# Kernel optimization log

Hardware: AMD Instinct MI355X
Metric: run time of the kernel (lower is better)

The kernel has to match this reference:

```python
import jax, jax.numpy as jnp
import numpy as np

B, N, K, D, H, L = 2, 2048, 256, 768, 256, 64
REL_PROP = 3
NUM_BUCKETS = 64


def _pair_scores(u, dist_feat, left_w, left_b, right_w, right_b, out_w, out_b):
    # OptFFpairs-style pairwise scorer: left(u)_i + right(u)_j + dist_emb -> relu -> out
    left = jnp.einsum('bkd,hd->bkh', u, left_w) + left_b    # [B,K,H]
    right = jnp.einsum('bkd,hd->bkh', u, right_w) + right_b  # [B,K,H]
    h = jax.nn.relu(left[:, :, None, :] + right[:, None, :, :] + dist_feat)  # [B,K,K,H]
    return jnp.einsum('bijh,lh->bijl', h, out_w) + out_b     # [B,K,K,L]


def setup_inputs():
    key = jax.random.key(0)
    ks = jax.random.split(key, 12)
    s = 0.02
    all_span_vecs = jax.random.normal(ks[0], (B, N, D), dtype=jnp.float32)
    span_vecs = jax.random.normal(ks[1], (B, K, D), dtype=jnp.float32)
    span_begin = jnp.sort(jax.random.randint(ks[2], (B, K), 0, 1000), axis=-1).astype(jnp.int32)
    span_end = (span_begin + jax.random.randint(ks[3], (B, K), 1, 16)).astype(jnp.int32)
    square_mask = jnp.ones((B, K, K), dtype=jnp.float32)
    span_lengths = jnp.full((B,), float(K), dtype=jnp.float32)
    prune_indices = jnp.stack([
        jnp.sort(jax.random.choice(jax.random.fold_in(ks[4], b), N, (K,), replace=False))
        for b in range(B)
    ]).astype(jnp.int32)
    return {
        'all_span_vecs': all_span_vecs, 'span_vecs': span_vecs,
        'span_begin': span_begin, 'span_end': span_end,
        'square_mask': square_mask, 'span_lengths': span_lengths,
        'prune_indices': prune_indices,
        'left_w': jax.random.normal(ks[5], (H, D)) * s, 'left_b': jnp.zeros((H,), jnp.float32),
        'right_w': jax.random.normal(ks[6], (H, D)) * s, 'right_b': jnp.zeros((H,), jnp.float32),
        'dist_emb': jax.random.normal(ks[7], (NUM_BUCKETS, H)) * s,
        'out_w': jax.random.normal(ks[8], (L, H)) * s, 'out_b': jnp.zeros((L,), jnp.float32),
        'A_w': jax.random.normal(ks[9], (D, L)) * s,
        'B_w': jax.random.normal(ks[10], (D, L)) * s,
        'gate_w': jax.random.normal(ks[11], (D, 2 * D)) * s, 'gate_b': jnp.zeros((D,), jnp.float32),
    }


def reference(all_span_vecs, span_vecs, span_begin, span_end, square_mask, span_lengths,
              prune_indices, left_w, left_b, right_w, right_b, dist_emb, out_w, out_b,
              A_w, B_w, gate_w, gate_b):
    # distance-bucket embedding of the span pair (span_pair_generator)
    dist = span_begin[:, None, :] - span_end[:, :, None]                 # [B,K,K]
    buckets = jnp.clip(jnp.abs(dist), 0, NUM_BUCKETS - 1)
    dist_feat = dist_emb[buckets]                                        # [B,K,K,H]
    inv_len = 1.0 / span_lengths[:, None, None]                          # [B,1,1]

    update = span_vecs
    scores = _pair_scores(update, dist_feat, left_w, left_b, right_w, right_b, out_w, out_b)
    for _ in range(REL_PROP):
        probs = jax.nn.sigmoid(scores) * square_mask[..., None]          # [B,K,K,L]
        # torch: (A(probs) * update.unsqueeze(-2)).sum(-3) -> sum over i (rows)
        ctxt1 = jnp.einsum('bijl,dl,bid->bjd', probs, A_w, update) * inv_len
        # torch: (B(probs) * update.unsqueeze(-3)).sum(-2) -> sum over j (cols)
        ctxt2 = jnp.einsum('bijl,dl,bjd->bid', probs, B_w, update) * inv_len
        c = ctxt1 + ctxt2
        # MyGate: sigmoid-gated convex combination of old state and context
        g = jax.nn.sigmoid(jnp.concatenate([update, c], axis=-1) @ gate_w.T + gate_b)
        update = g * update + (1.0 - g) * c
        scores = _pair_scores(update, dist_feat, left_w, left_b, right_w, right_b, out_w, out_b)

    # overwrite_spans: scatter updated filtered spans back into the full span tensor
    valid = jnp.arange(K)[None, :] < span_lengths[:, None]               # [B,K]
    old = jnp.take_along_axis(all_span_vecs, prune_indices[..., None], axis=1)
    vals = jnp.where(valid[..., None], update, old)
    bidx = jnp.arange(B)[:, None]
    new_all = all_span_vecs.at[bidx, prune_indices].set(vals)
    return new_all, update, scores
```

## Files before the change

kernel.cpp:

```cpp
#include <hip/hip_runtime.h>

#define B_ 2
#define N_ 2048
#define K_ 256
#define D_ 768
#define H_ 256
#define L_ 64
#define BK_ (B_*K_)

typedef __attribute__((ext_vector_type(8))) __bf16 bf16x8;
typedef __attribute__((ext_vector_type(8))) unsigned short ushort8;
typedef __attribute__((ext_vector_type(4))) unsigned short ushort4v;
typedef __attribute__((ext_vector_type(4))) float f32x4;

__device__ __forceinline__ float sigm(float x) { return 1.0f / (1.0f + __expf(-x)); }

__device__ __forceinline__ unsigned short f2b(float f) {
    union { float f; unsigned int u; } v; v.f = f;
    unsigned int u = v.u;
    return (unsigned short)((u + 0x7FFFu + ((u >> 16) & 1u)) >> 16);
}
__device__ __forceinline__ unsigned short f2bc(float f) {
    __bf16 h = (__bf16)f;
    return __builtin_bit_cast(unsigned short, h);
}
__device__ __forceinline__ float b2f(unsigned short us) {
    union { unsigned int u; float f; } v; v.u = ((unsigned int)us) << 16;
    return v.f;
}
__device__ __forceinline__ bf16x8 ldb(const unsigned short* p) {
    ushort8 v = *(const ushort8*)p;
    return __builtin_bit_cast(bf16x8, v);
}
__device__ __forceinline__ bf16x8 cvt8(const float* p) {
    float4 v0 = *(const float4*)p;
    float4 v1 = *(const float4*)(p + 4);
    ushort8 u;
    u[0] = f2b(v0.x); u[1] = f2b(v0.y); u[2] = f2b(v0.z); u[3] = f2b(v0.w);
    u[4] = f2b(v1.x); u[5] = f2b(v1.y); u[6] = f2b(v1.z); u[7] = f2b(v1.w);
    return __builtin_bit_cast(bf16x8, u);
}

__global__ __launch_bounds__(256) void conv_all(
    const float* __restrict__ lw, const float* __restrict__ rw,
    const float* __restrict__ ow, const float* __restrict__ gw,
    const float* __restrict__ aw, const float* __restrict__ bw,
    const float* __restrict__ sv,
    unsigned short* __restrict__ lwb, unsigned short* __restrict__ rwb,
    unsigned short* __restrict__ owb, unsigned short* __restrict__ gwb,
    unsigned short* __restrict__ wab, unsigned short* __restrict__ wbb,
    unsigned short* __restrict__ ub)
{
    int i4 = (blockIdx.x * 256 + threadIdx.x) * 4;
    const float* src; unsigned short* dst; int off;
    if      (i4 <  196608) { src = lw; dst = lwb; off = 0; }
    else if (i4 <  393216) { src = rw; dst = rwb; off = 196608; }
    else if (i4 <  409600) { src = ow; dst = owb; off = 393216; }
    else if (i4 < 1589248) { src = gw; dst = gwb; off = 409600; }
    else if (i4 < 1638400) { src = aw; dst = wab; off = 1589248; }
    else if (i4 < 1687552) { src = bw; dst = wbb; off = 1638400; }
    else if (i4 < 2080768) { src = sv; dst = ub;  off = 1687552; }
    else return;
    int j = i4 - off;
    float4 v = *(const float4*)&src[j];
    ushort4v p; p.x = f2b(v.x); p.y = f2b(v.y); p.z = f2b(v.z); p.w = f2b(v.w);
    *(ushort4v*)&dst[j] = p;
}

__global__ __launch_bounds__(64) void lr_mfma(
    const unsigned short* __restrict__ Ub,
    const unsigned short* __restrict__ lwb, const float* __restrict__ lb,
    const unsigned short* __restrict__ rwb, const float* __restrict__ rb,
    float* __restrict__ outL, float* __restrict__ outR)
{
    const int side = blockIdx.z;
    const unsigned short* __restrict__ W = side ? rwb : lwb;
    const float* __restrict__ bias = side ? rb : lb;
    float* __restrict__ outp = side ? outR : outL;
    const int r0 = blockIdx.x * 16, n0 = blockIdx.y * 64;
    const int lane = threadIdx.x;
    const int col = lane & 15, quad = lane >> 4;
    const unsigned short* arow = &Ub[(size_t)(r0 + col)*D_ + quad*8];
    f32x4 acc[4] = {};
    #pragma unroll 4
    for (int kc = 0; kc < D_; kc += 32) {
        bf16x8 a = ldb(arow + kc);
        #pragma unroll
        for (int nt = 0; nt < 4; ++nt) {
            bf16x8 bb = ldb(&W[(size_t)(n0 + nt*16 + col)*D_ + kc + quad*8]);
            acc[nt] = __builtin_amdgcn_mfma_f32_16x16x32_bf16(a, bb, acc[nt], 0, 0, 0);
        }
    }
    #pragma unroll
    for (int nt = 0; nt < 4; ++nt) {
        const int n = n0 + nt*16 + col;
        const float bv = bias[n];
        #pragma unroll
        for (int r = 0; r < 4; ++r) {
            const size_t idx = (size_t)(r0 + quad*4 + r)*H_ + n;
            outp[idx] = acc[nt][r] + bv;
        }
    }
}

__global__ __launch_bounds__(256, 1) void scores_v8(
    const float* __restrict__ leftb, const float* __restrict__ rightb,
    const int* __restrict__ span_begin, const int* __restrict__ span_end,
    const float* __restrict__ de, const unsigned short* __restrict__ owb,
    const float* __restrict__ out_b, const float* __restrict__ mask,
    float* __restrict__ S, unsigned short* __restrict__ Pt, int writeP)
{
    const int j0 = blockIdx.x * 64;
    const int i0 = blockIdx.y * 8;
    const int b  = blockIdx.z;
    const int tid = threadIdx.x;
    const int w = tid >> 6, lane = tid & 63, col = lane & 15, quad = lane >> 4;
    const int jrow = w*16 + col;

    __shared__ float sL[8][256];
    __shared__ float sT[64][68];
    __shared__ float sMask[8][64];
    __shared__ int   sBkt[8][64];

    #pragma unroll
    for (int q = 0; q < 2; ++q) {
        int p = tid + q*256;
        int ii = p >> 6, jj = p & 63;
        int d = span_begin[b*K_ + j0 + jj] - span_end[b*K_ + i0 + ii];
        if (d < 0) d = -d;
        sBkt[ii][jj] = d > 63 ? 63 : d;
        sMask[ii][jj] = mask[(size_t)(b*K_ + i0 + ii)*K_ + j0 + jj];
    }
    #pragma unroll
    for (int q = 0; q < 2; ++q) {
        int f = tid + q*256;
        int row = f >> 6, c4 = (f & 63) * 4;
        *(float4*)&sL[row][c4] = *(const float4*)&leftb[(size_t)(b*K_ + i0 + row)*H_ + c4];
    }
    __syncthreads();

    int deoff[8];
    #pragma unroll
    for (int i = 0; i < 8; ++i) deoff[i] = sBkt[i][jrow] * H_;

    const float* rrow = &rightb[(size_t)(b*K_ + j0 + jrow)*H_ + quad*8];

    f32x4 acc[8][4] = {};
    #pragma unroll
    for (int k = 0; k < 8; ++k) {
        const float4 r0 = *(const float4*)&rrow[k*32];
        const float4 r1 = *(const float4*)&rrow[k*32 + 4];
        bf16x8 bbk[4];
        #pragma unroll
        for (int lt = 0; lt < 4; ++lt)
            bbk[lt] = ldb(&owb[(size_t)(lt*16 + col)*H_ + k*32 + quad*8]);
        #pragma unroll
        for (int i = 0; i < 8; ++i) {
            const float* dr = &de[deoff[i] + k*32 + quad*8];
            const float4 d0 = *(const float4*)dr;
            const float4 d1 = *(const float4*)(dr + 4);
            const float* lr = &sL[i][k*32 + quad*8];
            const float4 l0 = *(const float4*)lr;
            const float4 l1 = *(const float4*)(lr + 4);
            bf16x8 a;
            a[0] = (__bf16)fmaxf(0.f, l0.x + r0.x + d0.x);
            a[1] = (__bf16)fmaxf(0.f, l0.y + r0.y + d0.y);
            a[2] = (__bf16)fmaxf(0.f, l0.z + r0.z + d0.z);
            a[3] = (__bf16)fmaxf(0.f, l0.w + r0.w + d0.w);
            a[4] = (__bf16)fmaxf(0.f, l1.x + r1.x + d1.x);
            a[5] = (__bf16)fmaxf(0.f, l1.y + r1.y + d1.y);
            a[6] = (__bf16)fmaxf(0.f, l1.z + r1.z + d1.z);
            a[7] = (__bf16)fmaxf(0.f, l1.w + r1.w + d1.w);
            #pragma unroll
            for (int lt = 0; lt < 4; ++lt)
                acc[i][lt] = __builtin_amdgcn_mfma_f32_16x16x32_bf16(a, bbk[lt], acc[i][lt], 0, 0, 0);
        }
    }

    float ob[4];
    #pragma unroll
    for (int lt = 0; lt < 4; ++lt) ob[lt] = out_b[lt*16 + col];

    #pragma unroll
    for (int i = 0; i < 8; ++i) {
        __syncthreads();
        #pragma unroll
        for (int lt = 0; lt < 4; ++lt)
            #pragma unroll
            for (int r = 0; r < 4; ++r)
                sT[w*16 + quad*4 + r][lt*16 + col] = acc[i][lt][r] + ob[lt];
        __syncthreads();
        const int jj = tid >> 2, seg = (tid & 3) * 16;
        const int j = j0 + jj, ii = i0 + i;
        if (writeP) {
            const float msk = sMask[i][jj];
            ushort8 o0, o1;
            #pragma unroll
            for (int e = 0; e < 8; ++e) {
                o0[e] = f2bc(sigm(sT[jj][seg + e]) * msk);
                o1[e] = f2bc(sigm(sT[jj][seg + 8 + e]) * msk);
            }
            unsigned short* dst = &Pt[(((size_t)b*K_ + j)*K_ + ii)*L_ + seg];
            *(ushort8*)&dst[0] = o0;
            *(ushort8*)&dst[8] = o1;
        } else {
            float* dst = &S[(((size_t)b*K_ + ii)*K_ + j)*L_ + seg];
            #pragma unroll
            for (int q2 = 0; q2 < 4; ++q2) {
                float4 v;
                v.x = sT[jj][seg + q2*4 + 0];
                v.y = sT[jj][seg + q2*4 + 1];
                v.z = sT[jj][seg + q2*4 + 2];
                v.w = sT[jj][seg + q2*4 + 3];
                *(float4*)&dst[q2*4] = v;
            }
        }
    }
}

__global__ __launch_bounds__(256) void ctxt_v2(
    const unsigned short* __restrict__ Pt, const float* __restrict__ U,
    const unsigned short* __restrict__ WAb, const unsigned short* __restrict__ WBb,
    const float* __restrict__ lens, float* __restrict__ cacc)
{
    const int bid = blockIdx.x;
    const int m0 = (bid & 15) << 4;
    const int t0 = ((bid >> 4) & 3) << 6;
    const int mode = (bid >> 6) & 1;
    const int b = bid >> 7;
    const unsigned short* __restrict__ Wb = mode ? WBb : WAb;
    const int tid = threadIdx.x;
    const int w = tid >> 6, lane = tid & 63, col = lane & 15, quad = lane >> 4;
    const int dbase = w * 192;

    __shared__ unsigned short sP[2][16][72];
    __shared__ float sU[2][768];

    bf16x8 bw[12][2];
    #pragma unroll
    for (int dt = 0; dt < 12; ++dt)
        #pragma unroll
        for (int kc = 0; kc < 2; ++kc)
            bw[dt][kc] = ldb(&Wb[(size_t)(dbase + dt*16 + col)*L_ + kc*32 + quad*8]);

    const bool doP = tid < 128, doU = tid < 192;
    const int prow = (tid & 127) >> 3, pseg = (tid & 7) * 8;
    size_t pbase, tstep;
    if (mode) { pbase = (((size_t)b*K_ + t0)*K_ + m0 + prow)*L_ + pseg; tstep = (size_t)K_*L_; }
    else      { pbase = (((size_t)b*K_ + m0 + prow)*K_ + t0)*L_ + pseg; tstep = (size_t)L_; }
    const size_t ubase = ((size_t)b*K_ + t0)*D_ + (size_t)(doU ? tid : 0)*4;

    ushort8 pv0, pv1; float4 uv0, uv1;
    if (doP) { pv0 = *(const ushort8*)&Pt[pbase];
               pv1 = *(const ushort8*)&Pt[pbase + tstep]; }
    if (doU) { uv0 = *(const float4*)&U[ubase];
               uv1 = *(const float4*)&U[ubase + D_]; }

    f32x4 acc[12] = {};

    #define CTXT_PHASE(BUFI, PV, UV, TOFF)                                        \
    {                                                                             \
        if (doP) *(ushort8*)&sP[BUFI][prow][pseg] = PV;                           \
        if (doU) *(float4*)&sU[BUFI][tid*4] = UV;                                 \
        if (t + (TOFF) < 64) {                                                    \
            if (doP) PV = *(const ushort8*)&Pt[pbase + (size_t)(t + (TOFF))*tstep]; \
            if (doU) UV = *(const float4*)&U[ubase + (size_t)(t + (TOFF))*D_];    \
        }                                                                         \
        __syncthreads();                                                          \
        bf16x8 a0 = ldb(&sP[BUFI][col][quad*8]);                                  \
        bf16x8 a1 = ldb(&sP[BUFI][col][32 + quad*8]);                             \
        _Pragma("unroll")                                                         \
        for (int dt = 0; dt < 12; ++dt) {                                         \
            f32x4 g = {0.f, 0.f, 0.f, 0.f};                                       \
            g = __builtin_amdgcn_mfma_f32_16x16x32_bf16(a0, bw[dt][0], g, 0, 0, 0); \
            g = __builtin_amdgcn_mfma_f32_16x16x32_bf16(a1, bw[dt][1], g, 0, 0, 0); \
            const float uu = sU[BUFI][dbase + dt*16 + col];                       \
            acc[dt] += g * uu;                                                    \
        }                                                                         \
        __syncthreads();                                                          \
    }

    for (int t = 0; t < 64; t += 2) {
        CTXT_PHASE(0, pv0, uv0, 2)
        CTXT_PHASE(1, pv1, uv1, 3)
    }
    #undef CTXT_PHASE

    const float inv_len = 1.0f / lens[b];
    #pragma unroll
    for (int dt = 0; dt < 12; ++dt)
        #pragma unroll
        for (int r = 0; r < 4; ++r) {
            const int m = m0 + quad*4 + r;
            atomicAdd(&cacc[((size_t)(b*K_) + m)*D_ + dbase + dt*16 + col],
                      acc[dt][r] * inv_len);
        }
}

__global__ __launch_bounds__(64) void gate_mfma(
    const unsigned short* __restrict__ Ub, const unsigned short* __restrict__ gwb,
    const float* __restrict__ gb,
    const float* __restrict__ Ucur, const float* __restrict__ Cc,
    float* __restrict__ Unext, unsigned short* __restrict__ Ubnext)
{
    const int r0 = blockIdx.x * 16, n0 = blockIdx.y * 64;
    const int lane = threadIdx.x;
    const int col = lane & 15, quad = lane >> 4;
    const unsigned short* arow_u = &Ub[(size_t)(r0 + col)*D_ + quad*8];
    const float* arow_c = &Cc[(size_t)(r0 + col)*D_ + quad*8];
    f32x4 acc[4] = {};
    #pragma unroll 4
    for (int kc = 0; kc < D_; kc += 32) {
        bf16x8 a = ldb(arow_u + kc);
        #pragma unroll
        for (int nt = 0; nt < 4; ++nt) {
            bf16x8 bb = ldb(&gwb[(size_t)(n0 + nt*16 + col)*(2*D_) + kc + quad*8]);
            acc[nt] = __builtin_amdgcn_mfma_f32_16x16x32_bf16(a, bb, acc[nt], 0, 0, 0);
        }
    }
    #pragma unroll 4
    for (int kc = 0; kc < D_; kc += 32) {
        bf16x8 a = cvt8(arow_c + kc);
        #pragma unroll
        for (int nt = 0; nt < 4; ++nt) {
            bf16x8 bb = ldb(&gwb[(size_t)(n0 + nt*16 + col)*(2*D_) + D_ + kc + quad*8]);
            acc[nt] = __builtin_amdgcn_mfma_f32_16x16x32_bf16(a, bb, acc[nt], 0, 0, 0);
        }
    }
    #pragma unroll
    for (int nt = 0; nt < 4; ++nt) {
        const int n = n0 + nt*16 + col;
        const float gbv = gb[n];
        #pragma unroll
        for (int r = 0; r < 4; ++r) {
            const size_t idx = (size_t)(r0 + quad*4 + r)*D_ + n;
            const float gg = sigm(acc[nt][r] + gbv);
            const float o = gg * Ucur[idx] + (1.f - gg) * Cc[idx];
            Unext[idx] = o;
            Ubnext[idx] = f2b(o);
        }
    }
}

__global__ __launch_bounds__(256) void scatter_kernel(
    const float* __restrict__ upd, const int* __restrict__ prune,
    const float* __restrict__ lens, float* __restrict__ out_all)
{
    const int blk = blockIdx.x;
    const int b = blk / K_, k = blk % K_;
    if ((float)k < lens[b]) {
        const int pi = prune[b*K_ + k];
        const int tid = threadIdx.x;
        if (tid < D_/4) {
            float4 v = *(const float4*)&upd[((size_t)b*K_ + k)*D_ + tid*4];
            *(float4*)&out_all[((size_t)b*N_ + pi)*D_ + tid*4] = v;
        }
    }
}

extern "C" void kernel_launch(void* const* d_in, const int* in_sizes, int n_in,
                              void* d_out, int out_size, void* d_ws, size_t ws_size,
                              hipStream_t stream) {
    (void)in_sizes; (void)n_in; (void)out_size; (void)ws_size;
    const float* all_span_vecs = (const float*)d_in[0];
    const float* span_vecs     = (const float*)d_in[1];
    const int*   span_begin    = (const int*)d_in[2];
    const int*   span_end      = (const int*)d_in[3];
    const float* mask          = (const float*)d_in[4];
    const float* lens          = (const float*)d_in[5];
    const int*   prune         = (const int*)d_in[6];
    const float* lw  = (const float*)d_in[7];
    const float* lb  = (const float*)d_in[8];
    const float* rw  = (const float*)d_in[9];
    const float* rb  = (const float*)d_in[10];
    const float* dist_emb = (const float*)d_in[11];
    const float* out_w    = (const float*)d_in[12];
    const float* out_b    = (const float*)d_in[13];
    const float* A_w = (const float*)d_in[14];
    const float* B_w = (const float*)d_in[15];
    const float* gw  = (const float*)d_in[16];
    const float* gb  = (const float*)d_in[17];

    float* out_all = (float*)d_out;
    float* out_upd = out_all + (size_t)B_*N_*D_;
    float* out_sc  = out_upd + (size_t)BK_*D_;

    float* ws     = (float*)d_ws;
    float* leftb  = ws;
    float* rightf = leftb + (size_t)BK_*H_;
    float* U0     = rightf + (size_t)BK_*H_;
    float* U1     = U0 + (size_t)BK_*D_;
    float* cbuf   = U1 + (size_t)BK_*D_;
    unsigned short* WAb = (unsigned short*)(cbuf + (size_t)BK_*D_);
    unsigned short* WBb = WAb + (size_t)D_*L_;
    unsigned short* lwb = WBb + (size_t)D_*L_;
    unsigned short* rwb = lwb + (size_t)H_*D_;
    unsigned short* owb = rwb + (size_t)H_*D_;
    unsigned short* gwb = owb + (size_t)L_*H_;
    unsigned short* Ub0 = gwb + (size_t)D_*2*D_;
    unsigned short* Ub1 = Ub0 + (size_t)BK_*D_;
    unsigned short* Pt  = Ub1 + (size_t)BK_*D_;

    hipMemcpyAsync(out_all, all_span_vecs, sizeof(float)*(size_t)B_*N_*D_,
                   hipMemcpyDeviceToDevice, stream);

    dim3 blk256(256), blk64(64);
    conv_all<<<dim3(2032), blk256, 0, stream>>>(lw, rw, out_w, gw, A_w, B_w, span_vecs,
                                                lwb, rwb, owb, gwb, WAb, WBb, Ub0);
    lr_mfma<<<dim3(BK_/16, H_/64, 2), blk64, 0, stream>>>(Ub0, lwb, lb, rwb, rb, leftb, rightf);
    scores_v8<<<dim3(K_/64, K_/8, B_), blk256, 0, stream>>>(leftb, rightf, span_begin, span_end,
                                                            dist_emb, owb, out_b, mask,
                                                            out_sc, Pt, 1);
    const float* Ucur = span_vecs;
    const unsigned short* Ubcur = Ub0;
    float* nexts[3] = {U0, U1, out_upd};
    unsigned short* nextsUb[3] = {Ub1, Ub0, Ub1};
    for (int it = 0; it < 3; ++it) {
        hipMemsetAsync(cbuf, 0, sizeof(float)*(size_t)BK_*D_, stream);
        ctxt_v2<<<dim3(256), blk256, 0, stream>>>(Pt, Ucur, WAb, WBb, lens, cbuf);
        gate_mfma<<<dim3(BK_/16, D_/64), blk64, 0, stream>>>(Ubcur, gwb, gb,
                                                             Ucur, cbuf, nexts[it], nextsUb[it]);
        Ucur = nexts[it];
        Ubcur = nextsUb[it];
        lr_mfma<<<dim3(BK_/16, H_/64, 2), blk64, 0, stream>>>(Ubcur, lwb, lb, rwb, rb, leftb, rightf);
        scores_v8<<<dim3(K_/64, K_/8, B_), blk256, 0, stream>>>(leftb, rightf, span_begin, span_end,
                                                                dist_emb, owb, out_b, mask,
                                                                out_sc, Pt, it == 2 ? 0 : 1);
    }
    scatter_kernel<<<dim3(BK_), blk256, 0, stream>>>(out_upd, prune, lens, out_all);
}
```

Before: 468.3 us.

## Split ctxt reduction across more blocks and load operands directly to registers

The context kernel now splits the t-reduction into 32-step chunks instead of 64, doubling the grid to 512 blocks so more CUs are busy. The shared-memory staging and both __syncthreads per step are removed. Each lane now loads its own MFMA A-operand fragments and U values straight from global memory into registers, double-buffered. The cost is twice as many atomicAdds into the context buffer, redundant U loads across waves, and higher register pressure under the new launch_bounds occupancy hint.

Result: slower. 609.7 us (+30.2%).

```diff
diff --git a/kernel.cpp b/kernel.cpp
--- a/kernel.cpp
+++ b/kernel.cpp
@@ -218,24 +218,21 @@
     }
 }
 
-__global__ __launch_bounds__(256) void ctxt_v2(
+__global__ __launch_bounds__(256, 2) void ctxt_v3(
     const unsigned short* __restrict__ Pt, const float* __restrict__ U,
     const unsigned short* __restrict__ WAb, const unsigned short* __restrict__ WBb,
     const float* __restrict__ lens, float* __restrict__ cacc)
 {
     const int bid = blockIdx.x;
     const int m0 = (bid & 15) << 4;
-    const int t0 = ((bid >> 4) & 3) << 6;
-    const int mode = (bid >> 6) & 1;
-    const int b = bid >> 7;
+    const int t0 = ((bid >> 4) & 7) << 5;
+    const int mode = (bid >> 7) & 1;
+    const int b = bid >> 8;
     const unsigned short* __restrict__ Wb = mode ? WBb : WAb;
     const int tid = threadIdx.x;
     const int w = tid >> 6, lane = tid & 63, col = lane & 15, quad = lane >> 4;
     const int dbase = w * 192;
 
-    __shared__ unsigned short sP[2][16][72];
-    __shared__ float sU[2][768];
-
     bf16x8 bw[12][2];
     #pragma unroll
     for (int dt = 0; dt < 12; ++dt)
@@ -243,48 +240,50 @@
         for (int kc = 0; kc < 2; ++kc)
             bw[dt][kc] = ldb(&Wb[(size_t)(dbase + dt*16 + col)*L_ + kc*32 + quad*8]);
 
-    const bool doP = tid < 128, doU = tid < 192;
-    const int prow = (tid & 127) >> 3, pseg = (tid & 7) * 8;
     size_t pbase, tstep;
-    if (mode) { pbase = (((size_t)b*K_ + t0)*K_ + m0 + prow)*L_ + pseg; tstep = (size_t)K_*L_; }
-    else      { pbase = (((size_t)b*K_ + m0 + prow)*K_ + t0)*L_ + pseg; tstep = (size_t)L_; }
-    const size_t ubase = ((size_t)b*K_ + t0)*D_ + (size_t)(doU ? tid : 0)*4;
-
-    ushort8 pv0, pv1; float4 uv0, uv1;
-    if (doP) { pv0 = *(const ushort8*)&Pt[pbase];
-               pv1 = *(const ushort8*)&Pt[pbase + tstep]; }
-    if (doU) { uv0 = *(const float4*)&U[ubase];
-               uv1 = *(const float4*)&U[ubase + D_]; }
+    if (mode) { pbase = (((size_t)b*K_ + t0)*K_ + m0 + col)*L_ + quad*8; tstep = (size_t)K_*L_; }
+    else      { pbase = (((size_t)b*K_ + m0 + col)*K_ + t0)*L_ + quad*8; tstep = (size_t)L_; }
+    const float* ubase = &U[((size_t)b*K_ + t0)*D_ + dbase + col];
+
+    ushort8 pA0 = *(const ushort8*)&Pt[pbase];
+    ushort8 pA1 = *(const ushort8*)&Pt[pbase + 32];
+    ushort8 pB0 = *(const ushort8*)&Pt[pbase + tstep];
+    ushort8 pB1 = *(const ushort8*)&Pt[pbase + tstep + 32];
+    float uA[12], uB[12];
+    #pragma unroll
+    for (int dt = 0; dt < 12; ++dt) { uA[dt] = ubase[dt*16]; uB[dt] = ubase[D_ + dt*16]; }
 
     f32x4 acc[12] = {};
 
-    #define CTXT_PHASE(BUFI, PV, UV, TOFF)                                        \
+    #define CTXT_STEP(P0, P1, UU, TNEXT)                                          \
     {                                                                             \
-        if (doP) *(ushort8*)&sP[BUFI][prow][pseg] = PV;                           \
-        if (doU) *(float4*)&sU[BUFI][tid*4] = UV;                                 \
-        if (t + (TOFF) < 64) {                                                    \
-            if (doP) PV = *(const ushort8*)&Pt[pbase + (size_t)(t + (TOFF))*tstep]; \
-            if (doU) UV = *(const float4*)&U[ubase + (size_t)(t + (TOFF))*D_];    \
+        bf16x8 a0 = __builtin_bit_cast(bf16x8, P0);                               \
+        bf16x8 a1 = __builtin_bit_cast(bf16x8, P1);                               \
+        float uu[12];                                                             \
+        _Pragma("unroll")                                                         \
+        for (int dt = 0; dt < 12; ++dt) uu[dt] = UU[dt];                          \
+        if ((TNEXT) < 32) {                                                       \
+            const size_t pa = pbase + (size_t)(TNEXT)*tstep;                      \
+            P0 = *(const ushort8*)&Pt[pa];                                        \
+            P1 = *(const ushort8*)&Pt[pa + 32];                                   \
+            const float* ua = ubase + (size_t)(TNEXT)*D_;                         \
+            _Pragma("unroll")                                                     \
+            for (int dt = 0; dt < 12; ++dt) UU[dt] = ua[dt*16];                   \
         }                                                                         \
-        __syncthreads();                                                          \
-        bf16x8 a0 = ldb(&sP[BUFI][col][quad*8]);                                  \
-        bf16x8 a1 = ldb(&sP[BUFI][col][32 + quad*8]);                             \
         _Pragma("unroll")                                                         \
         for (int dt = 0; dt < 12; ++dt) {                                         \
             f32x4 g = {0.f, 0.f, 0.f, 0.f};                                       \
             g = __builtin_amdgcn_mfma_f32_16x16x32_bf16(a0, bw[dt][0], g, 0, 0, 0); \
             g = __builtin_amdgcn_mfma_f32_16x16x32_bf16(a1, bw[dt][1], g, 0, 0, 0); \
-            const float uu = sU[BUFI][dbase + dt*16 + col];                       \
-            acc[dt] += g * uu;                                                    \
+            acc[dt] += g * uu[dt];                                                \
         }                                                                         \
-        __syncthreads();                                                          \
-    }
-
-    for (int t = 0; t < 64; t += 2) {
-        CTXT_PHASE(0, pv0, uv0, 2)
-        CTXT_PHASE(1, pv1, uv1, 3)
-    }
-    #undef CTXT_PHASE
+    }
+
+    for (int t = 0; t < 32; t += 2) {
+        CTXT_STEP(pA0, pA1, uA, t + 2)
+        CTXT_STEP(pB0, pB1, uB, t + 3)
+    }
+    #undef CTXT_STEP
 
     const float inv_len = 1.0f / lens[b];
     #pragma unroll
@@ -417,7 +416,7 @@
     unsigned short* nextsUb[3] = {Ub1, Ub0, Ub1};
     for (int it = 0; it < 3; ++it) {
         hipMemsetAsync(cbuf, 0, sizeof(float)*(size_t)BK_*D_, stream);
-        ctxt_v2<<<dim3(256), blk256, 0, stream>>>(Pt, Ucur, WAb, WBb, lens, cbuf);
+        ctxt_v3<<<dim3(512), blk256, 0, stream>>>(Pt, Ucur, WAb, WBb, lens, cbuf);
         gate_mfma<<<dim3(BK_/16, D_/64), blk64, 0, stream>>>(Ubcur, gwb, gb,
                                                              Ucur, cbuf, nexts[it], nextsUb[it]);
         Ucur = nexts[it];
```

## Split context kernel across more blocks and waves with single-sync double buffering

Applied to the files above, without the earlier changes.

The context-accumulation kernel now runs 512 blocks of 512 threads. Each wave covers 96 feature columns instead of 192, and the reduction dimension is split into 8 chunks of 32 instead of 4 chunks of 64. The loop keeps the double buffer but drops the second barrier per step; the double buffer keeps it race-free. The aim is higher occupancy, less register pressure and fewer barriers, paid for with twice as many atomic adds into the context buffer.

Result: faster. 449.2 us (-4.1%).

```diff
diff --git a/kernel.cpp b/kernel.cpp
--- a/kernel.cpp
+++ b/kernel.cpp
@@ -218,77 +218,69 @@
     }
 }
 
-__global__ __launch_bounds__(256) void ctxt_v2(
+__global__ __launch_bounds__(512, 4) void ctxt_v4(
     const unsigned short* __restrict__ Pt, const float* __restrict__ U,
     const unsigned short* __restrict__ WAb, const unsigned short* __restrict__ WBb,
     const float* __restrict__ lens, float* __restrict__ cacc)
 {
     const int bid = blockIdx.x;
     const int m0 = (bid & 15) << 4;
-    const int t0 = ((bid >> 4) & 3) << 6;
-    const int mode = (bid >> 6) & 1;
-    const int b = bid >> 7;
+    const int t0 = ((bid >> 4) & 7) << 5;
+    const int mode = (bid >> 7) & 1;
+    const int b = bid >> 8;
     const unsigned short* __restrict__ Wb = mode ? WBb : WAb;
     const int tid = threadIdx.x;
     const int w = tid >> 6, lane = tid & 63, col = lane & 15, quad = lane >> 4;
-    const int dbase = w * 192;
+    const int dbase = w * 96;
 
     __shared__ unsigned short sP[2][16][72];
     __shared__ float sU[2][768];
 
-    bf16x8 bw[12][2];
-    #pragma unroll
-    for (int dt = 0; dt < 12; ++dt)
+    bf16x8 bw[6][2];
+    #pragma unroll
+    for (int dt = 0; dt < 6; ++dt)
         #pragma unroll
         for (int kc = 0; kc < 2; ++kc)
             bw[dt][kc] = ldb(&Wb[(size_t)(dbase + dt*16 + col)*L_ + kc*32 + quad*8]);
 
-    const bool doP = tid < 128, doU = tid < 192;
+    const bool doP = tid < 128;
+    const bool doU = (tid >= 128) && (tid < 320);
     const int prow = (tid & 127) >> 3, pseg = (tid & 7) * 8;
+    const int ucol = (tid - 128) * 4;
     size_t pbase, tstep;
     if (mode) { pbase = (((size_t)b*K_ + t0)*K_ + m0 + prow)*L_ + pseg; tstep = (size_t)K_*L_; }
     else      { pbase = (((size_t)b*K_ + m0 + prow)*K_ + t0)*L_ + pseg; tstep = (size_t)L_; }
-    const size_t ubase = ((size_t)b*K_ + t0)*D_ + (size_t)(doU ? tid : 0)*4;
-
-    ushort8 pv0, pv1; float4 uv0, uv1;
-    if (doP) { pv0 = *(const ushort8*)&Pt[pbase];
-               pv1 = *(const ushort8*)&Pt[pbase + tstep]; }
-    if (doU) { uv0 = *(const float4*)&U[ubase];
-               uv1 = *(const float4*)&U[ubase + D_]; }
-
-    f32x4 acc[12] = {};
-
-    #define CTXT_PHASE(BUFI, PV, UV, TOFF)                                        \
-    {                                                                             \
-        if (doP) *(ushort8*)&sP[BUFI][prow][pseg] = PV;                           \
-        if (doU) *(float4*)&sU[BUFI][tid*4] = UV;                                 \
-        if (t + (TOFF) < 64) {                                                    \
-            if (doP) PV = *(const ushort8*)&Pt[pbase + (size_t)(t + (TOFF))*tstep]; \
-            if (doU) UV = *(const float4*)&U[ubase + (size_t)(t + (TOFF))*D_];    \
-        }                                                                         \
-        __syncthreads();                                                          \
-        bf16x8 a0 = ldb(&sP[BUFI][col][quad*8]);                                  \
-        bf16x8 a1 = ldb(&sP[BUFI][col][32 + quad*8]);                             \
-        _Pragma("unroll")                                                         \
-        for (int dt = 0; dt < 12; ++dt) {                                         \
-            f32x4 g = {0.f, 0.f, 0.f, 0.f};                                       \
-            g = __builtin_amdgcn_mfma_f32_16x16x32_bf16(a0, bw[dt][0], g, 0, 0, 0); \
-            g = __builtin_amdgcn_mfma_f32_16x16x32_bf16(a1, bw[dt][1], g, 0, 0, 0); \
-            const float uu = sU[BUFI][dbase + dt*16 + col];                       \
-            acc[dt] += g * uu;                                                    \
-        }                                                                         \
-        __syncthreads();                                                          \
-    }
-
-    for (int t = 0; t < 64; t += 2) {
-        CTXT_PHASE(0, pv0, uv0, 2)
-        CTXT_PHASE(1, pv1, uv1, 3)
-    }
-    #undef CTXT_PHASE
+
+    ushort8 pv; float4 uv;
+    if (doP) pv = *(const ushort8*)&Pt[pbase];
+    if (doU) uv = *(const float4*)&U[((size_t)b*K_ + t0)*D_ + ucol];
+
+    f32x4 acc[6] = {};
+    for (int t = 0; t < 32; ++t) {
+        unsigned short (*bp)[72] = sP[t & 1];
+        float* bu = sU[t & 1];
+        if (doP) *(ushort8*)&bp[prow][pseg] = pv;
+        if (doU) *(float4*)&bu[ucol] = uv;
+        if (t < 31) {
+            if (doP) pv = *(const ushort8*)&Pt[pbase + (size_t)(t + 1)*tstep];
+            if (doU) uv = *(const float4*)&U[((size_t)b*K_ + t0 + t + 1)*D_ + ucol];
+        }
+        __syncthreads();
+        bf16x8 a0 = ldb(&bp[col][quad*8]);
+        bf16x8 a1 = ldb(&bp[col][32 + quad*8]);
+        #pragma unroll
+        for (int dt = 0; dt < 6; ++dt) {
+            f32x4 g = {0.f, 0.f, 0.f, 0.f};
+            g = __builtin_amdgcn_mfma_f32_16x16x32_bf16(a0, bw[dt][0], g, 0, 0, 0);
+            g = __builtin_amdgcn_mfma_f32_16x16x32_bf16(a1, bw[dt][1], g, 0, 0, 0);
+            const float uu = bu[dbase + dt*16 + col];
+            acc[dt] += g * uu;
+        }
+    }
 
     const float inv_len = 1.0f / lens[b];
     #pragma unroll
-    for (int dt = 0; dt < 12; ++dt)
+    for (int dt = 0; dt < 6; ++dt)
         #pragma unroll
         for (int r = 0; r < 4; ++r) {
             const int m = m0 + quad*4 + r;
@@ -404,7 +396,7 @@
     hipMemcpyAsync(out_all, all_span_vecs, sizeof(float)*(size_t)B_*N_*D_,
                    hipMemcpyDeviceToDevice, stream);
 
-    dim3 blk256(256), blk64(64);
+    dim3 blk256(256), blk64(64), blk512(512);
     conv_all<<<dim3(2032), blk256, 0, stream>>>(lw, rw, out_w, gw, A_w, B_w, span_vecs,
                                                 lwb, rwb, owb, gwb, WAb, WBb, Ub0);
     lr_mfma<<<dim3(BK_/16, H_/64, 2), blk64, 0, stream>>>(Ub0, lwb, lb, rwb, rb, leftb, rightf);
@@ -417,7 +409,7 @@
     unsigned short* nextsUb[3] = {Ub1, Ub0, Ub1};
     for (int it = 0; it < 3; ++it) {
         hipMemsetAsync(cbuf, 0, sizeof(float)*(size_t)BK_*D_, stream);
-        ctxt_v2<<<dim3(256), blk256, 0, stream>>>(Pt, Ucur, WAb, WBb, lens, cbuf);
+        ctxt_v4<<<dim3(512), blk512, 0, stream>>>(Pt, Ucur, WAb, WBb, lens, cbuf);
         gate_mfma<<<dim3(BK_/16, D_/64), blk64, 0, stream>>>(Ubcur, gwb, gb,
                                                              Ucur, cbuf, nexts[it], nextsUb[it]);
         Ucur = nexts[it];
```
